# Kernel tuning notes

Hardware: AMD Instinct MI355X
Metric: run time of the kernel (lower is better)

The kernel has to match this reference:

```python
import jax, jax.numpy as jnp
import numpy as np

B, L, D = 32, 2048, 512  # D == num_clusters == dim (required by the module's own shape algebra)
CONC = 100.0
EPS = 1e-12


def setup_inputs() -> dict:
    key = jax.random.key(0)
    k1, k2 = jax.random.split(key)
    x = jax.random.normal(k1, (B, L, D), dtype=jnp.float32)
    # torch.rand(dim, num_clusters)
    centroids = jax.random.uniform(k2, (D, D), dtype=jnp.float32)
    return {"x": x, "centroids": centroids}


def reference(x, centroids):
    # _forward: per-feature power scale over the token axis
    scale = jnp.mean(x * x, axis=1, keepdims=True)            # (B,1,D)
    direction = x / jnp.maximum(scale, EPS)                    # (B,L,D)

    # conv (1x1 Conv1d): weight[k,d] = 2*conc*centroids[k,d], bias[k] = -conc*||centroids[k,:]||
    bias = -CONC * jnp.linalg.norm(centroids, axis=1)          # (K,)
    logits = jnp.einsum('bld,kd->blk', direction, 2.0 * CONC * centroids) + bias  # (B,L,K)
    # original softmaxes over dim=1 of (B,L,K) -> the token axis L
    a = jax.nn.softmax(logits, axis=1)                         # (B,L,K)

    # VLAD: sum_l a[b,l,k] * (direction[b,l,:] - centroids[k,:])
    # rewritten as two small contractions (no (B,L,K,D) intermediate)
    vlad = jnp.einsum('blk,bld->bkd', a, direction)            # (B,K,D)
    vlad = vlad - jnp.sum(a, axis=1)[..., None] * centroids    # (B,K,D)

    out = scale * vlad                                         # (B,1,D)*(B,K,D)
    return jnp.mean(out, axis=1)                               # (B,D)
```

## Files before the change

### kernel.cpp

```cpp
#include <hip/hip_runtime.h>
#include <math.h>

#define B_ 32
#define L_ 2048
#define D_ 512
#define K_ 512
#define CONC_ 100.0f
#define EPS_ 1e-12f
#define LSPLIT 16
#define EXPSCALE 1.44269504088896f

typedef __attribute__((ext_vector_type(8))) _Float16 f16x8;
typedef __attribute__((ext_vector_type(4))) _Float16 f16x4;
typedef __attribute__((ext_vector_type(4))) float f32x4;

enum : size_t {
  O_MEANC = 0,
  O_PM    = O_MEANC + D_,
  O_PS    = O_PM + (size_t)B_*LSPLIT*K_,
  O_SCP   = O_PS + (size_t)B_*LSPLIT*K_,
  O_WXP   = O_SCP + (size_t)B_*8*D_,
  O_CFB   = O_WXP + (size_t)B_*16*D_,
  O_X16   = O_CFB + (size_t)B_*K_*D_/2,
  O_P16   = O_X16 + (size_t)B_*L_*D_/2,
  WS_FLOATS = O_P16 + (size_t)B_*L_*K_/2
};

__device__ __forceinline__ void gl2lds16(const void* gsrc, void* lds) {
  __builtin_amdgcn_global_load_lds(
      (const __attribute__((address_space(1))) void*)gsrc,
      (__attribute__((address_space(3))) void*)lds, 16, 0, 0);
}

__global__ void k_meanc(const float* __restrict__ cent, float* ws) {
  int d = blockIdx.x * 256 + threadIdx.x;
  float s = 0.f;
  for (int k = 0; k < K_; ++k) s += cent[(size_t)k * D_ + d];
  ws[O_MEANC + d] = s * (1.f / K_);
}

__global__ void k_sqacc(const float* __restrict__ x, float* ws) {
  int b = blockIdx.x, dc = blockIdx.y, lc = blockIdx.z;
  int d = dc * 256 + threadIdx.x;
  size_t base = ((size_t)b * L_ + lc * 256) * D_ + d;
  const float* xb = x + base;
  _Float16* x16b = reinterpret_cast<_Float16*>(ws + O_X16) + base;
  float acc = 0.f;
  for (int l = 0; l < 256; ++l) {
    float v = xb[(size_t)l * D_];
    acc += v * v;
    x16b[(size_t)l * D_] = (_Float16)v;
  }
  ws[O_SCP + ((size_t)b * 8 + lc) * D_ + d] = acc;
}

__global__ void k_cfb(const float* __restrict__ cent, float* ws) {
  int b = blockIdx.y;
  int f = (blockIdx.x * 256 + threadIdx.x) * 4;
  int d = f & (D_ - 1);
  float4 c = *reinterpret_cast<const float4*>(cent + f);
  float4 s4 = {0.f, 0.f, 0.f, 0.f};
  const float* scp = ws + O_SCP + (size_t)b * 8 * D_ + d;
#pragma unroll
  for (int lc = 0; lc < 8; ++lc) {
    float4 p = *reinterpret_cast<const float4*>(scp + lc * D_);
    s4.x += p.x; s4.y += p.y; s4.z += p.z; s4.w += p.w;
  }
  const float sc = 2.f * CONC_ * EXPSCALE;
  f16x4 h;
  h[0] = (_Float16)(c.x * sc / fmaxf(s4.x * (1.f / L_), EPS_));
  h[1] = (_Float16)(c.y * sc / fmaxf(s4.y * (1.f / L_), EPS_));
  h[2] = (_Float16)(c.z * sc / fmaxf(s4.z * (1.f / L_), EPS_));
  h[3] = (_Float16)(c.w * sc / fmaxf(s4.w * (1.f / L_), EPS_));
  *reinterpret_cast<f16x4*>(
      reinterpret_cast<_Float16*>(ws + O_CFB) + (size_t)b * K_ * D_ + f) = h;
}

__global__ __launch_bounds__(256, 3) void k_gemm16(float* ws) {
  const int id = blockIdx.x;
  const int xcd = id & 7;
  const int r = id >> 3;
  const int b = xcd + ((r >> 6) << 3);
  const int lk = r & 63;
  const int lchunk = lk & 15;
  const int l0 = lchunk * 128;
  const int k0 = (lk >> 4) * 128;

  __shared__ _Float16 As[128 * 64];
  __shared__ _Float16 Bs[128 * 64];
  const int tid = threadIdx.x;
  const int lane = tid & 63;
  const int w = tid >> 6;
  const int wm = w >> 1, wn = w & 1;

  const _Float16* xb16 = reinterpret_cast<const _Float16*>(ws + O_X16) +
                         (size_t)b * L_ * D_;
  const _Float16* cfb = reinterpret_cast<const _Float16*>(ws + O_CFB) +
                        (size_t)b * K_ * D_;

  f32x4 acc[4][4] = {};

#pragma unroll
  for (int d0 = 0; d0 < D_; d0 += 64) {
#pragma unroll
    for (int rr = 0; rr < 4; ++rr) {
      int u = rr * 256 + tid;
      int row = u >> 3, j = u & 7;
      int sc = ((j ^ (row & 7)) << 3);
      gl2lds16(xb16 + (size_t)(l0 + row) * D_ + d0 + sc, As + (size_t)u * 8);
    }
#pragma unroll
    for (int rr = 0; rr < 4; ++rr) {
      int u = rr * 256 + tid;
      int row = u >> 3, j = u & 7;
      int sc = ((j ^ (row & 7)) << 3);
      gl2lds16(cfb + (size_t)(k0 + row) * D_ + d0 + sc, Bs + (size_t)u * 8);
    }
    __syncthreads();

#pragma unroll
    for (int kk = 0; kk < 2; ++kk) {
      f16x8 af[4], bfr[4];
#pragma unroll
      for (int mi = 0; mi < 4; ++mi) {
        int row = wm * 64 + mi * 16 + (lane & 15);
        int slot = kk * 4 + (lane >> 4);
        int sw = slot ^ (row & 7);
        af[mi] = *reinterpret_cast<const f16x8*>(
            reinterpret_cast<const char*>(As) + row * 128 + sw * 16);
      }
#pragma unroll
      for (int ni = 0; ni < 4; ++ni) {
        int row = wn * 64 + ni * 16 + (lane & 15);
        int slot = kk * 4 + (lane >> 4);
        int sw = slot ^ (row & 7);
        bfr[ni] = *reinterpret_cast<const f16x8*>(
            reinterpret_cast<const char*>(Bs) + row * 128 + sw * 16);
      }
#pragma unroll
      for (int mi = 0; mi < 4; ++mi)
#pragma unroll
        for (int ni = 0; ni < 4; ++ni)
          acc[mi][ni] = __builtin_amdgcn_mfma_f32_16x16x32_f16(
              af[mi], bfr[ni], acc[mi][ni], 0, 0, 0);
    }
    __syncthreads();
  }

  float* red = reinterpret_cast<float*>(As);
  float* red2 = red + 256;
  float pm[4], ps[4];
#pragma unroll
  for (int ni = 0; ni < 4; ++ni) {
    float m = -INFINITY;
#pragma unroll
    for (int mi = 0; mi < 4; ++mi)
#pragma unroll
      for (int j = 0; j < 4; ++j) m = fmaxf(m, acc[mi][ni][j]);
    m = fmaxf(m, __shfl_xor(m, 16));
    m = fmaxf(m, __shfl_xor(m, 32));
    pm[ni] = m;
  }
  if (lane < 16) {
#pragma unroll
    for (int ni = 0; ni < 4; ++ni)
      red[wm * 128 + wn * 64 + ni * 16 + lane] = pm[ni];
  }
  __syncthreads();
#pragma unroll
  for (int ni = 0; ni < 4; ++ni) {
    int idx = wn * 64 + ni * 16 + (lane & 15);
    pm[ni] = fmaxf(red[idx], red[128 + idx]);
  }
  _Float16* pg = reinterpret_cast<_Float16*>(ws + O_P16) + (size_t)b * K_ * L_;
#pragma unroll
  for (int ni = 0; ni < 4; ++ni) {
    int kc = k0 + wn * 64 + ni * 16 + (lane & 15);
    float s = 0.f;
#pragma unroll
    for (int mi = 0; mi < 4; ++mi) {
      int lr = l0 + wm * 64 + mi * 16 + (lane >> 4) * 4;
      f16x4 ev;
#pragma unroll
      for (int j = 0; j < 4; ++j) {
        float e = exp2f(acc[mi][ni][j] - pm[ni]);
        s += e;
        ev[j] = (_Float16)e;
      }
      *reinterpret_cast<f16x4*>(pg + (size_t)kc * L_ + lr) = ev;
    }
    s += __shfl_xor(s, 16);
    s += __shfl_xor(s, 32);
    ps[ni] = s;
  }
  if (lane < 16) {
#pragma unroll
    for (int ni = 0; ni < 4; ++ni)
      red2[wm * 128 + wn * 64 + ni * 16 + lane] = ps[ni];
  }
  __syncthreads();
  if (w < 2 && lane < 16) {
#pragma unroll
    for (int ni = 0; ni < 4; ++ni) {
      int idx = wn * 64 + ni * 16 + lane;
      float mg = fmaxf(red[idx], red[128 + idx]);
      float sg = red2[idx] + red2[128 + idx];
      size_t o = ((size_t)b * LSPLIT + lchunk) * K_ + k0 + idx;
      ws[O_PM + o] = mg;
      ws[O_PS + o] = sg;
    }
  }
}

__global__ __launch_bounds__(256) void k_wsumwx(float* ws) {
  int b = blockIdx.x, ch = blockIdx.y;
  int l0 = ch * 128;
  __shared__ float Al[512];
  __shared__ float wacc[16][128];
  __shared__ float wl[128];
  int tid = threadIdx.x;

  for (int kk = tid; kk < K_; kk += 256) {
    float pmv[LSPLIT], psv[LSPLIT];
    float M = -INFINITY;
#pragma unroll
    for (int c = 0; c < LSPLIT; ++c) {
      pmv[c] = ws[O_PM + ((size_t)b * LSPLIT + c) * K_ + kk];
      psv[c] = ws[O_PS + ((size_t)b * LSPLIT + c) * K_ + kk];
      M = fmaxf(M, pmv[c]);
    }
    float S = 0.f;
#pragma unroll
    for (int c = 0; c < LSPLIT; ++c) S += psv[c] * exp2f(pmv[c] - M);
    Al[kk] = exp2f(pmv[ch] - M) / S;
  }
  __syncthreads();

  const _Float16* pt = reinterpret_cast<const _Float16*>(ws + O_P16) +
                       (size_t)b * K_ * L_ + l0;
  int lpart = tid & 15, kslice = tid >> 4;
  float a8[8] = {0.f, 0.f, 0.f, 0.f, 0.f, 0.f, 0.f, 0.f};
  for (int k = kslice * 32; k < kslice * 32 + 32; ++k) {
    float ak = Al[k];
    f16x8 v = *reinterpret_cast<const f16x8*>(pt + (size_t)k * L_ + lpart * 8);
#pragma unroll
    for (int i = 0; i < 8; ++i) a8[i] += ak * (float)v[i];
  }
#pragma unroll
  for (int i = 0; i < 8; ++i) wacc[kslice][lpart * 8 + i] = a8[i];
  __syncthreads();
  if (tid < 128) {
    float s = 0.f;
#pragma unroll
    for (int sl = 0; sl < 16; ++sl) s += wacc[sl][tid];
    wl[tid] = s;
  }
  __syncthreads();

  const _Float16* x16b = reinterpret_cast<const _Float16*>(ws + O_X16) +
                         (size_t)(b * L_ + l0) * D_;
  int half = tid >> 7;
  int dd = (tid & 127) * 4;
  float4 a4 = {0.f, 0.f, 0.f, 0.f};
  for (int l = half * 64; l < half * 64 + 64; ++l) {
    float wgt = wl[l];
    f16x4 xv = *reinterpret_cast<const f16x4*>(x16b + (size_t)l * D_ + dd);
    a4.x += wgt * (float)xv[0];
    a4.y += wgt * (float)xv[1];
    a4.z += wgt * (float)xv[2];
    a4.w += wgt * (float)xv[3];
  }
  float* wxp = ws + O_WXP + ((size_t)b * 16 + ch) * D_ + dd;
  if (half == 0) {
    wxp[0] = a4.x; wxp[1] = a4.y; wxp[2] = a4.z; wxp[3] = a4.w;
  }
  __syncthreads();
  if (half == 1) {
    wxp[0] += a4.x; wxp[1] += a4.y; wxp[2] += a4.z; wxp[3] += a4.w;
  }
}

__global__ void k_final(const float* ws, float* out) {
  int i = blockIdx.x * 256 + threadIdx.x;
  int b = i >> 9, d = i & (D_ - 1);
  float scale = 0.f;
#pragma unroll
  for (int lc = 0; lc < 8; ++lc)
    scale += ws[O_SCP + ((size_t)b * 8 + lc) * D_ + d];
  float wx = 0.f;
#pragma unroll
  for (int c = 0; c < 16; ++c)
    wx += ws[O_WXP + ((size_t)b * 16 + c) * D_ + d];
  float sc = scale * (1.f / L_);
  float inv = 1.f / fmaxf(sc, EPS_);
  out[i] = sc * (inv * wx * (1.f / K_) - ws[O_MEANC + d]);
}

extern "C" void kernel_launch(void* const* d_in, const int* in_sizes, int n_in,
                              void* d_out, int out_size, void* d_ws, size_t ws_size,
                              hipStream_t stream) {
  const float* x = (const float*)d_in[0];
  const float* cent = (const float*)d_in[1];
  float* out = (float*)d_out;
  float* ws = (float*)d_ws;

  k_sqacc<<<dim3(B_, D_ / 256, 8), 256, 0, stream>>>(x, ws);
  k_meanc<<<2, 256, 0, stream>>>(cent, ws);
  k_cfb<<<dim3(K_ * D_ / 1024, B_), 256, 0, stream>>>(cent, ws);
  k_gemm16<<<2048, 256, 0, stream>>>(ws);
  k_wsumwx<<<dim3(B_, LSPLIT), 256, 0, stream>>>(ws);
  k_final<<<B_ * D_ / 256, 256, 0, stream>>>(ws, out);
}
```

Before: 148.0 us.

## Store softmax exponentials as FP8 e4m3 and merge centroid-mean into cfb kernel

The unnormalized exponentials passed between the GEMM kernel and the weighted-sum kernel are now packed as FP8 e4m3 instead of FP16, halving that intermediate's write and read traffic. The small centroid-mean kernel is folded into the cfb kernel as two extra blocks, removing one launch. FP8 quantization of the probabilities loses precision and may break tolerance, and the software fp8 conversion adds ALU work on both sides.

```diff
diff --git a/kernel.cpp b/kernel.cpp
--- a/kernel.cpp
+++ b/kernel.cpp
@@ -1,4 +1,5 @@
 #include <hip/hip_runtime.h>
+#include <hip/hip_fp8.h>
 #include <math.h>
 
 #define B_ 32
@@ -22,21 +23,14 @@
   O_WXP   = O_SCP + (size_t)B_*8*D_,
   O_CFB   = O_WXP + (size_t)B_*16*D_,
   O_X16   = O_CFB + (size_t)B_*K_*D_/2,
-  O_P16   = O_X16 + (size_t)B_*L_*D_/2,
-  WS_FLOATS = O_P16 + (size_t)B_*L_*K_/2
+  O_P8    = O_X16 + (size_t)B_*L_*D_/2,
+  WS_FLOATS = O_P8 + (size_t)B_*K_*L_/4
 };
 
 __device__ __forceinline__ void gl2lds16(const void* gsrc, void* lds) {
   __builtin_amdgcn_global_load_lds(
       (const __attribute__((address_space(1))) void*)gsrc,
       (__attribute__((address_space(3))) void*)lds, 16, 0, 0);
-}
-
-__global__ void k_meanc(const float* __restrict__ cent, float* ws) {
-  int d = blockIdx.x * 256 + threadIdx.x;
-  float s = 0.f;
-  for (int k = 0; k < K_; ++k) s += cent[(size_t)k * D_ + d];
-  ws[O_MEANC + d] = s * (1.f / K_);
 }
 
 __global__ void k_sqacc(const float* __restrict__ x, float* ws) {
@@ -54,9 +48,17 @@
   ws[O_SCP + ((size_t)b * 8 + lc) * D_ + d] = acc;
 }
 
-__global__ void k_cfb(const float* __restrict__ cent, float* ws) {
-  int b = blockIdx.y;
-  int f = (blockIdx.x * 256 + threadIdx.x) * 4;
+__global__ void k_cfbm(const float* __restrict__ cent, float* ws) {
+  int blk = blockIdx.x, tid = threadIdx.x;
+  if (blk >= 8192) {
+    int d = (blk - 8192) * 256 + tid;
+    float s = 0.f;
+    for (int k = 0; k < K_; ++k) s += cent[(size_t)k * D_ + d];
+    ws[O_MEANC + d] = s * (1.f / K_);
+    return;
+  }
+  int b = blk >> 8;
+  int f = ((blk & 255) * 256 + tid) * 4;
   int d = f & (D_ - 1);
   float4 c = *reinterpret_cast<const float4*>(cent + f);
   float4 s4 = {0.f, 0.f, 0.f, 0.f};
@@ -172,7 +174,7 @@
     int idx = wn * 64 + ni * 16 + (lane & 15);
     pm[ni] = fmaxf(red[idx], red[128 + idx]);
   }
-  _Float16* pg = reinterpret_cast<_Float16*>(ws + O_P16) + (size_t)b * K_ * L_;
+  char* pg = reinterpret_cast<char*>(ws + O_P8) + (size_t)b * K_ * L_;
 #pragma unroll
   for (int ni = 0; ni < 4; ++ni) {
     int kc = k0 + wn * 64 + ni * 16 + (lane & 15);
@@ -180,14 +182,15 @@
 #pragma unroll
     for (int mi = 0; mi < 4; ++mi) {
       int lr = l0 + wm * 64 + mi * 16 + (lane >> 4) * 4;
-      f16x4 ev;
+      unsigned int pk = 0;
 #pragma unroll
       for (int j = 0; j < 4; ++j) {
         float e = exp2f(acc[mi][ni][j] - pm[ni]);
         s += e;
-        ev[j] = (_Float16)e;
+        __hip_fp8_e4m3 q(e);
+        pk |= (unsigned int)(q.__x) << (8 * j);
       }
-      *reinterpret_cast<f16x4*>(pg + (size_t)kc * L_ + lr) = ev;
+      *reinterpret_cast<unsigned int*>(pg + (size_t)kc * L_ + lr) = pk;
     }
     s += __shfl_xor(s, 16);
     s += __shfl_xor(s, 32);
@@ -236,15 +239,25 @@
   }
   __syncthreads();
 
-  const _Float16* pt = reinterpret_cast<const _Float16*>(ws + O_P16) +
-                       (size_t)b * K_ * L_ + l0;
+  const char* pt = reinterpret_cast<const char*>(ws + O_P8) +
+                   (size_t)b * K_ * L_ + l0;
   int lpart = tid & 15, kslice = tid >> 4;
   float a8[8] = {0.f, 0.f, 0.f, 0.f, 0.f, 0.f, 0.f, 0.f};
   for (int k = kslice * 32; k < kslice * 32 + 32; ++k) {
     float ak = Al[k];
-    f16x8 v = *reinterpret_cast<const f16x8*>(pt + (size_t)k * L_ + lpart * 8);
-#pragma unroll
-    for (int i = 0; i < 8; ++i) a8[i] += ak * (float)v[i];
+    uint2 v = *reinterpret_cast<const uint2*>(pt + (size_t)k * L_ + lpart * 8);
+#pragma unroll
+    for (int i = 0; i < 4; ++i) {
+      __hip_fp8_e4m3 q;
+      q.__x = (__hip_fp8_storage_t)((v.x >> (8 * i)) & 0xff);
+      a8[i] += ak * (float)q;
+    }
+#pragma unroll
+    for (int i = 0; i < 4; ++i) {
+      __hip_fp8_e4m3 q;
+      q.__x = (__hip_fp8_storage_t)((v.y >> (8 * i)) & 0xff);
+      a8[4 + i] += ak * (float)q;
+    }
   }
 #pragma unroll
   for (int i = 0; i < 8; ++i) wacc[kslice][lpart * 8 + i] = a8[i];
@@ -305,8 +318,7 @@
   float* ws = (float*)d_ws;
 
   k_sqacc<<<dim3(B_, D_ / 256, 8), 256, 0, stream>>>(x, ws);
-  k_meanc<<<2, 256, 0, stream>>>(cent, ws);
-  k_cfb<<<dim3(K_ * D_ / 1024, B_), 256, 0, stream>>>(cent, ws);
+  k_cfbm<<<8194, 256, 0, stream>>>(cent, ws);
   k_gemm16<<<2048, 256, 0, stream>>>(ws);
   k_wsumwx<<<dim3(B_, LSPLIT), 256, 0, stream>>>(ws);
   k_final<<<B_ * D_ / 256, 256, 0, stream>>>(ws, out);
```

Measured after the change: 131.2 us. -11.3%, faster.
